# Performance work log

Measured on AMD Instinct MI355X. Metric: run time of the kernel, lower is better.

## Reference

```python
import jax, jax.numpy as jnp
import numpy as np
from jax import lax

P = 10  # patch_size


def _conv(x, w, b, pad):
    y = lax.conv_general_dilated(x, w, (1, 1), [(pad, pad), (pad, pad)],
                                 dimension_numbers=('NCHW', 'OIHW', 'NCHW'))
    return y + b[None, :, None, None]


def setup_inputs() -> dict:
    key = jax.random.key(0)
    ks = jax.random.split(key, 9)
    B, Cin, H, W = 8, 3, 320, 320
    classes = 2
    p2 = P * P
    s = 0.05
    return {
        'x': jax.random.normal(ks[0], (B, Cin, H, W), jnp.float32),
        'w_conv1': jax.random.normal(ks[1], (64, Cin, 7, 7), jnp.float32) * s,
        'b_conv1': jax.random.normal(ks[2], (64,), jnp.float32) * s,
        'w_conv2': jax.random.normal(ks[3], (classes, 64, 3, 3), jnp.float32) * s,
        'b_conv2': jax.random.normal(ks[4], (classes,), jnp.float32) * s,
        'w_fm': jax.random.normal(ks[5], (classes, Cin, 1, 1), jnp.float32) * s,
        'b_fm': jax.random.normal(ks[6], (classes,), jnp.float32) * s,
        'w_lin1': jax.random.normal(ks[7], (2 * p2, p2), jnp.float32) * s,  # torch Linear [out,in]
        'w_lin2': jax.random.normal(ks[8], (p2, 2 * p2), jnp.float32) * s,
    }


def reference(x, w_conv1, b_conv1, w_conv2, b_conv2, w_fm, b_fm, w_lin1, w_lin2):
    p = P
    ini = _conv(_conv(x, w_conv1, b_conv1, 3), w_conv2, b_conv2, 1)  # [B,classes,H,W]
    fea = _conv(x, w_fm, b_fm, 0) / 4.0                              # [B,classes,H,W]
    B, C, H, W = ini.shape
    L = (H // p) * (W // p)

    def unfold(t):  # non-overlapping patches: [B,C,H,W] -> [B,C,L,p*p]
        t = t.reshape(B, C, H // p, p, W // p, p)
        return t.transpose(0, 1, 2, 4, 3, 5).reshape(B, C, L, p * p)

    def trans(t):  # Linear(p2->2p2) -> Linear(2p2->p2) -> ReLU, per patch
        h = jnp.einsum('bclp,qp->bclq', t, w_lin1)
        return jax.nn.relu(jnp.einsum('bclq,pq->bclp', h, w_lin2))

    ui = trans(unfold(ini))   # [B,C,L,p2]
    uf = trans(unfold(fea))   # [B,C,L,p2]
    att = jnp.einsum('bclp,bcmp->bclm', ui, uf) / (p * p)  # [B,C,L,L]
    return att
```

## Files before the change

kernel.cpp:

```cpp
#include <hip/hip_runtime.h>

#define WS_M      0
#define WS_K      10000
#define WS_BETA   12646
#define WS_W9     12664
#define WS_BT     13150
#define WS_INI    16384
#define WS_UIT    (16384 + 1638400)
#define WS_UFT    (16384 + 2*1638400)

typedef short bf16x8 __attribute__((ext_vector_type(8)));
typedef float f32x4  __attribute__((ext_vector_type(4)));

__device__ inline ushort f2bf(float f) {
    unsigned u = __float_as_uint(f);
    unsigned r = (u + 0x7fffu + ((u >> 16) & 1u)) >> 16;
    return (ushort)r;
}

__global__ __launch_bounds__(256) void k_prep(const float* __restrict__ wl1,
                                              const float* __restrict__ wl2,
                                              const float* __restrict__ wc1,
                                              const float* __restrict__ bc1,
                                              const float* __restrict__ wc2,
                                              const float* __restrict__ bc2,
                                              float* __restrict__ ws) {
    int blk = blockIdx.x;
    int t = threadIdx.x;
    if (blk < 40) {
        int idx = blk * 256 + t;
        if (idx < 10000) {
            int p = idx / 100, r = idx % 100;
            float s = 0.f;
            for (int q = 0; q < 200; ++q)
                s += wl2[p * 200 + q] * wl1[q * 100 + r];
            ws[WS_M + r * 100 + p] = s;
        }
        return;
    }
    __shared__ float swc1[9408];
    __shared__ float swc2[1152];
    __shared__ float sBeta[18];
    for (int i = t; i < 9408; i += 256) swc1[i] = wc1[i];
    for (int i = t; i < 1152; i += 256) swc2[i] = wc2[i];
    __syncthreads();
    if (blk < 43) {
        int base = (blk - 40) * 882;
        for (int ii = t; ii < 882; ii += 256) {
            int idx = base + ii;
            int v = idx % 7; int t1 = idx / 7;
            int u = t1 % 7;  int t2 = t1 / 7;
            int ci = t2 % 3; int t3 = t2 / 3;
            int b = t3 % 3;  int t4 = t3 / 3;
            int a = t4 % 3;  int c = t4 / 3;
            float s = 0.f;
            for (int c64 = 0; c64 < 64; ++c64)
                s += swc2[((c * 64 + c64) * 3 + a) * 3 + b] *
                     swc1[((c64 * 3 + ci) * 7 + u) * 7 + v];
            ws[WS_K + idx] = s;
        }
        if (blk == 40) {
            if (t < 18) {
                int b = t % 3; int a = (t / 3) % 3; int c = t / 9;
                float s = 0.f;
                for (int c64 = 0; c64 < 64; ++c64)
                    s += swc2[((c * 64 + c64) * 3 + a) * 3 + b] * bc1[c64];
                sBeta[t] = s; ws[WS_BETA + t] = s;
            }
            __syncthreads();
            if (t < 2) {
                float s = bc2[t];
                for (int j2 = 0; j2 < 9; ++j2) s += sBeta[t * 9 + j2];
                ws[WS_BT + t] = s;
            }
        }
    } else {
        int idx = (blk - 43) * 243 + t;
        if (t < 243) {
            int dx = idx % 9; int t1 = idx / 9;
            int dy = t1 % 9;  int t2 = t1 / 9;
            int ci = t2 % 3;  int c = t2 / 3;
            float s = 0.f;
            for (int a = 0; a < 3; ++a) {
                int u = dy - a; if (u < 0 || u > 6) continue;
                for (int b = 0; b < 3; ++b) {
                    int v = dx - b; if (v < 0 || v > 6) continue;
                    for (int c64 = 0; c64 < 64; ++c64)
                        s += swc2[((c * 64 + c64) * 3 + a) * 3 + b] *
                             swc1[((c64 * 3 + ci) * 7 + u) * 7 + v];
                }
            }
            ws[WS_W9 + idx] = s;
        }
    }
}

__global__ __launch_bounds__(256) void k_convb(const float* __restrict__ x,
                                               const float* __restrict__ bc2,
                                               const float* __restrict__ ws,
                                               float* __restrict__ ini) {
    __shared__ float sx[3][40][40];
    int bid = blockIdx.x;
    int t = threadIdx.x;
    if (bid < 800) {
        int b = bid / 100, by = (bid / 10) % 10, bx = bid % 10;
        int gh0 = by * 32, gw0 = bx * 32;
        for (int idx = t; idx < 3 * 40 * 40; idx += 256) {
            int ci = idx / 1600;
            int rem = idx - ci * 1600;
            int rr = rem / 40, cc = rem - rr * 40;
            int gh = gh0 - 4 + rr, gw = gw0 - 4 + cc;
            float v = 0.f;
            if ((unsigned)gh < 320u && (unsigned)gw < 320u)
                v = x[(b * 3 + ci) * 102400 + gh * 320 + gw];
            sx[ci][rr][cc] = v;
        }
        __syncthreads();
        const float* W9g = ws + WS_W9;
        const float* Btg = ws + WS_BT;
        int r = t >> 3, cg = t & 7;
        int h = gh0 + r, w0c = gw0 + cg * 4;
        float acc0[4], acc1[4];
        float bt0 = Btg[0], bt1 = Btg[1];
        #pragma unroll
        for (int j = 0; j < 4; ++j) { acc0[j] = bt0; acc1[j] = bt1; }
        #pragma unroll
        for (int ci = 0; ci < 3; ++ci) {
            #pragma unroll
            for (int dy = 0; dy < 9; ++dy) {
                const float* xr = &sx[ci][r + dy][cg * 4];
                float4 xa = *(const float4*)(xr);
                float4 xb = *(const float4*)(xr + 4);
                float4 xc = *(const float4*)(xr + 8);
                float xv[12] = {xa.x, xa.y, xa.z, xa.w,
                                xb.x, xb.y, xb.z, xb.w,
                                xc.x, xc.y, xc.z, xc.w};
                #pragma unroll
                for (int dx = 0; dx < 9; ++dx) {
                    float w0t = W9g[ci * 81 + dy * 9 + dx];
                    float w1t = W9g[243 + ci * 81 + dy * 9 + dx];
                    #pragma unroll
                    for (int j = 0; j < 4; ++j) {
                        acc0[j] += w0t * xv[dx + j];
                        acc1[j] += w1t * xv[dx + j];
                    }
                }
            }
        }
        size_t obase = (size_t)(b * 2) * 102400 + h * 320 + w0c;
        bool edge = (by == 0) | (by == 9) | (bx == 0) | (bx == 9);
        if (!edge) {
            *(float4*)&ini[obase] = make_float4(acc0[0], acc0[1], acc0[2], acc0[3]);
            *(float4*)&ini[obase + 102400] = make_float4(acc1[0], acc1[1], acc1[2], acc1[3]);
        } else {
            bool rring = (h == 0) | (h == 319);
            #pragma unroll
            for (int j = 0; j < 4; ++j) {
                int w = w0c + j;
                if (!rring && w != 0 && w != 319) {
                    ini[obase + j] = acc0[j];
                    ini[obase + 102400 + j] = acc1[j];
                }
            }
        }
        return;
    }
    int witem = (bid - 800) * 4 + (t >> 6);
    int lane = t & 63;
    int b = witem / 1276, j = witem % 1276;
    int h, w;
    if (j < 320)      { h = 0;           w = j; }
    else if (j < 640) { h = 319;         w = j - 320; }
    else if (j < 958) { h = 1 + j - 640; w = 0; }
    else              { h = 1 + j - 958; w = 319; }
    const float* K    = ws + WS_K;
    const float* Beta = ws + WS_BETA;
    float acc0 = 0.f, acc1 = 0.f;
    #pragma unroll
    for (int rep = 0; rep < 3; ++rep) {
        int e = lane + rep * 64;
        if (e < 189) {
            int a = e / 63;    int rem  = e - a * 63;
            int bb = rem / 21; int rem2 = rem - bb * 21;
            int ci = rem2 / 7; int u = rem2 - ci * 7;
            int hh0 = h + a - 1;
            int ww0 = w + bb - 1;
            bool abv = ((unsigned)hh0 < 320u) & ((unsigned)ww0 < 320u);
            if (abv && ci == 0 && u == 0) {
                acc0 += Beta[a * 3 + bb];
                acc1 += Beta[9 + a * 3 + bb];
            }
            int hx = hh0 + u - 3;
            if (abv && (unsigned)hx < 320u) {
                const float* Kc = K + (a * 9 + bb * 3 + ci) * 49 + u * 7;
                const float* xr = x + (b * 3 + ci) * 102400 + hx * 320;
                #pragma unroll
                for (int v = 0; v < 7; ++v) {
                    int wx = ww0 + v - 3;
                    if ((unsigned)wx < 320u) {
                        float xv = xr[wx];
                        acc0 += Kc[v] * xv;
                        acc1 += Kc[1323 + v] * xv;
                    }
                }
            }
        }
    }
    #pragma unroll
    for (int off = 32; off > 0; off >>= 1) {
        acc0 += __shfl_down(acc0, off, 64);
        acc1 += __shfl_down(acc1, off, 64);
    }
    if (lane == 0) {
        size_t pb = (size_t)(b * 2) * 102400 + h * 320 + w;
        ini[pb] = acc0 + bc2[0];
        ini[pb + 102400] = acc1 + bc2[1];
    }
}

#define SPS 68
__global__ __launch_bounds__(256) void k_trans(const float* __restrict__ ini,
                                               const float* __restrict__ x,
                                               const float* __restrict__ wfm,
                                               const float* __restrict__ bfm,
                                               const float* __restrict__ ws,
                                               ushort* __restrict__ uiL,
                                               ushort* __restrict__ ufL) {
    __shared__ float sM[100 * 50];
    __shared__ float sP[100 * SPS];
    int bc = blockIdx.x;
    int lg = blockIdx.y;
    int zz = blockIdx.z;
    int mode = zz >> 1, pg = zz & 1;
    ushort* outL = mode ? ufL : uiL;
    int t = threadIdx.x;
    const float* Mt = ws + WS_M;
    for (int i = t; i < 5000; i += 256) {
        int r = i / 50, p = i % 50;
        sM[i] = Mt[r * 100 + pg * 50 + p];
    }
    int b = bc >> 1, c = bc & 1;
    int row0 = lg * 20;
    if (mode == 0) {
        for (int e = t; e < 6400; e += 256) {
            int irow = e / 320, col = e % 320;
            int off = (row0 + irow) * 320 + col;
            float val = ini[bc * 102400 + off];
            int li = (irow / 10) * 32 + col / 10;
            int r  = (irow % 10) * 10 + col % 10;
            sP[r * SPS + li] = val;
        }
    } else {
        float wf0 = wfm[c * 3 + 0], wf1 = wfm[c * 3 + 1], wf2 = wfm[c * 3 + 2];
        float bf = bfm[c];
        for (int e = t; e < 6400; e += 256) {
            int irow = e / 320, col = e % 320;
            int off = (row0 + irow) * 320 + col;
            float val = (bf + x[(b * 3 + 0) * 102400 + off] * wf0
                            + x[(b * 3 + 1) * 102400 + off] * wf1
                            + x[(b * 3 + 2) * 102400 + off] * wf2) * 0.25f;
            int li = (irow / 10) * 32 + col / 10;
            int r  = (irow % 10) * 10 + col % 10;
            sP[r * SPS + li] = val;
        }
    }
    if (pg == 1) {
        for (int e = t; e < 64 * 7; e += 256) {
            int l = lg * 64 + e / 7, q = e % 7;
            *(uint2*)&outL[((size_t)bc * 1024 + l) * 128 + 100 + q * 4] = make_uint2(0u, 0u);
        }
    }
    __syncthreads();
    if (t < 200) {
        int py = t / 8;
        int lx = t % 8;
        int p0 = py * 2, lo = lx * 8;
        float acc[2][8];
        #pragma unroll
        for (int i = 0; i < 2; ++i)
            #pragma unroll
            for (int j = 0; j < 8; ++j) acc[i][j] = 0.f;
        for (int r = 0; r < 100; ++r) {
            float2 a  = *(const float2*)&sM[r * 50 + p0];
            float4 b0 = *(const float4*)&sP[r * SPS + lo];
            float4 b1 = *(const float4*)&sP[r * SPS + lo + 4];
            float av[2] = {a.x, a.y};
            float bv[8] = {b0.x, b0.y, b0.z, b0.w, b1.x, b1.y, b1.z, b1.w};
            #pragma unroll
            for (int i = 0; i < 2; ++i)
                #pragma unroll
                for (int j = 0; j < 8; ++j)
                    acc[i][j] += av[i] * bv[j];
        }
        int pbase = pg * 50 + p0;
        #pragma unroll
        for (int j = 0; j < 8; ++j) {
            int l = lg * 64 + lo + j;
            unsigned v0 = f2bf(fmaxf(acc[0][j], 0.f));
            unsigned v1 = f2bf(fmaxf(acc[1][j], 0.f));
            *(unsigned*)&outL[((size_t)bc * 1024 + l) * 128 + pbase] = v0 | (v1 << 16);
        }
    }
}

__global__ __launch_bounds__(256) void k_att(const ushort* __restrict__ ui,
                                             const ushort* __restrict__ uf,
                                             float* __restrict__ out) {
    int bc   = blockIdx.z;
    int row0 = blockIdx.y * 128, col0 = blockIdx.x * 128;
    int wave = threadIdx.x >> 6, lane = threadIdx.x & 63;
    int r0 = row0 + (wave >> 1) * 64;
    int c0 = col0 + (wave & 1) * 64;
    int m = lane & 15, quad = lane >> 4;
    const ushort* ub = ui + (size_t)bc * 1024 * 128;
    const ushort* vb = uf + (size_t)bc * 1024 * 128;
    f32x4 acc[4][4];
    #pragma unroll
    for (int i = 0; i < 4; ++i)
        #pragma unroll
        for (int j = 0; j < 4; ++j)
            acc[i][j] = (f32x4){0.f, 0.f, 0.f, 0.f};
    #pragma unroll
    for (int k0 = 0; k0 < 128; k0 += 32) {
        bf16x8 af[4], bfr[4];
        #pragma unroll
        for (int i = 0; i < 4; ++i)
            af[i] = *(const bf16x8*)&ub[(size_t)(r0 + i * 16 + m) * 128 + k0 + quad * 8];
        #pragma unroll
        for (int j = 0; j < 4; ++j)
            bfr[j] = *(const bf16x8*)&vb[(size_t)(c0 + j * 16 + m) * 128 + k0 + quad * 8];
        #pragma unroll
        for (int i = 0; i < 4; ++i)
            #pragma unroll
            for (int j = 0; j < 4; ++j)
                acc[i][j] = __builtin_amdgcn_mfma_f32_16x16x32_bf16(af[i], bfr[j], acc[i][j], 0, 0, 0);
    }
    #pragma unroll
    for (int i = 0; i < 4; ++i) {
        #pragma unroll
        for (int r = 0; r < 4; ++r) {
            int row = r0 + i * 16 + quad * 4 + r;
            float* o = out + ((size_t)bc * 1024 + row) * 1024;
            #pragma unroll
            for (int j = 0; j < 4; ++j)
                o[c0 + j * 16 + m] = acc[i][j][r] * 0.01f;
        }
    }
}

extern "C" void kernel_launch(void* const* d_in, const int* in_sizes, int n_in,
                              void* d_out, int out_size, void* d_ws, size_t ws_size,
                              hipStream_t stream) {
    const float* x       = (const float*)d_in[0];
    const float* w_conv1 = (const float*)d_in[1];
    const float* b_conv1 = (const float*)d_in[2];
    const float* w_conv2 = (const float*)d_in[3];
    const float* b_conv2 = (const float*)d_in[4];
    const float* w_fm    = (const float*)d_in[5];
    const float* b_fm    = (const float*)d_in[6];
    const float* w_lin1  = (const float*)d_in[7];
    const float* w_lin2  = (const float*)d_in[8];
    float* out = (float*)d_out;
    float* ws  = (float*)d_ws;
    ushort* uiL = (ushort*)(ws + WS_UIT);
    ushort* ufL = (ushort*)(ws + WS_UFT);

    k_prep<<<45, 256, 0, stream>>>(w_lin1, w_lin2, w_conv1, b_conv1, w_conv2, b_conv2, ws);
    k_convb<<<3352, 256, 0, stream>>>(x, b_conv2, ws, ws + WS_INI);
    k_trans<<<dim3(16, 16, 4), 256, 0, stream>>>(ws + WS_INI, x, w_fm, b_fm, ws, uiL, ufL);
    k_att<<<dim3(8, 8, 16), 256, 0, stream>>>(uiL, ufL, out);
}
```

Before: 170.3 us.

## Fuse all stages into one persistent cooperative kernel with grid syncs

Replaces the four-kernel launch sequence with a single persistent cooperative kernel that runs the prep, conv, patch-transform and attention stages in turn, separated by grid-wide barriers. Each stage loops over its work items with a grid-stride loop, and shared memory is shared between stages through a union. The goal is to remove per-launch overhead and inter-kernel gaps. The cost is that grid syncs add their own barrier latency, occupancy is capped at three blocks per CU, and the fewer resident blocks may run some stages with less parallelism. The original kernels stay as a fallback if the cooperative launch fails.

```diff
diff --git a/kernel.cpp b/kernel.cpp
--- a/kernel.cpp
+++ b/kernel.cpp
@@ -1,4 +1,7 @@
 #include <hip/hip_runtime.h>
+#include <hip/hip_cooperative_groups.h>
+
+namespace cg = cooperative_groups;
 
 #define WS_M      0
 #define WS_K      10000
@@ -16,6 +19,341 @@
     unsigned u = __float_as_uint(f);
     unsigned r = (u + 0x7fffu + ((u >> 16) & 1u)) >> 16;
     return (ushort)r;
+}
+
+#define SPS 68
+
+__global__ __launch_bounds__(256, 3) void k_all(
+    const float* __restrict__ x,
+    const float* __restrict__ wl1, const float* __restrict__ wl2,
+    const float* __restrict__ wc1, const float* __restrict__ bc1,
+    const float* __restrict__ wc2, const float* __restrict__ bc2,
+    const float* __restrict__ wfm, const float* __restrict__ bfm,
+    float* __restrict__ ws, float* __restrict__ out)
+{
+    union alignas(16) SMem {
+        struct { float sx[3][40][40]; float sW9[486]; float sBt[2]; } conv;
+        struct { float sM[5000]; float sP[100 * SPS]; } trans;
+        struct { float swc1[9408]; float swc2[1152]; float sBeta[18]; } prep;
+    };
+    __shared__ SMem sm;
+
+    const int blk = blockIdx.x, t = threadIdx.x, nblk = gridDim.x;
+    float*  Mt   = ws + WS_M;
+    float*  Kw   = ws + WS_K;
+    float*  Beta = ws + WS_BETA;
+    float*  W9   = ws + WS_W9;
+    float*  Bt   = ws + WS_BT;
+    float*  ini  = ws + WS_INI;
+    ushort* uiL  = (ushort*)(ws + WS_UIT);
+    ushort* ufL  = (ushort*)(ws + WS_UFT);
+
+    if (blk < 40) {
+        int idx = blk * 256 + t;
+        if (idx < 10000) {
+            int p = idx / 100, r = idx % 100;
+            float s = 0.f;
+            for (int q = 0; q < 200; ++q)
+                s += wl2[p * 200 + q] * wl1[q * 100 + r];
+            Mt[r * 100 + p] = s;
+        }
+    } else if (blk < 45) {
+        for (int i = t; i < 9408; i += 256) sm.prep.swc1[i] = wc1[i];
+        for (int i = t; i < 1152; i += 256) sm.prep.swc2[i] = wc2[i];
+        __syncthreads();
+        if (blk < 43) {
+            int base = (blk - 40) * 882;
+            for (int ii = t; ii < 882; ii += 256) {
+                int idx = base + ii;
+                int v = idx % 7; int t1 = idx / 7;
+                int u = t1 % 7;  int t2 = t1 / 7;
+                int ci = t2 % 3; int t3 = t2 / 3;
+                int b = t3 % 3;  int t4 = t3 / 3;
+                int a = t4 % 3;  int c = t4 / 3;
+                float s = 0.f;
+                for (int c64 = 0; c64 < 64; ++c64)
+                    s += sm.prep.swc2[((c * 64 + c64) * 3 + a) * 3 + b] *
+                         sm.prep.swc1[((c64 * 3 + ci) * 7 + u) * 7 + v];
+                Kw[idx] = s;
+            }
+            if (blk == 40) {
+                if (t < 18) {
+                    int b = t % 3; int a = (t / 3) % 3; int c = t / 9;
+                    float s = 0.f;
+                    for (int c64 = 0; c64 < 64; ++c64)
+                        s += sm.prep.swc2[((c * 64 + c64) * 3 + a) * 3 + b] * bc1[c64];
+                    sm.prep.sBeta[t] = s; Beta[t] = s;
+                }
+                __syncthreads();
+                if (t < 2) {
+                    float s = bc2[t];
+                    for (int j2 = 0; j2 < 9; ++j2) s += sm.prep.sBeta[t * 9 + j2];
+                    Bt[t] = s;
+                }
+            }
+        } else {
+            int idx = (blk - 43) * 243 + t;
+            if (t < 243) {
+                int dx = idx % 9; int t1 = idx / 9;
+                int dy = t1 % 9;  int t2 = t1 / 9;
+                int ci = t2 % 3;  int c = t2 / 3;
+                float s = 0.f;
+                for (int a = 0; a < 3; ++a) {
+                    int u = dy - a; if (u < 0 || u > 6) continue;
+                    for (int b = 0; b < 3; ++b) {
+                        int v = dx - b; if (v < 0 || v > 6) continue;
+                        for (int c64 = 0; c64 < 64; ++c64)
+                            s += sm.prep.swc2[((c * 64 + c64) * 3 + a) * 3 + b] *
+                                 sm.prep.swc1[((c64 * 3 + ci) * 7 + u) * 7 + v];
+                    }
+                }
+                W9[idx] = s;
+            }
+        }
+    }
+    cg::this_grid().sync();
+
+    for (int u = blk; u < 3352; u += nblk) {
+        if (u < 800) {
+            int b = u / 100, by = (u / 10) % 10, bx = u % 10;
+            int gh0 = by * 32, gw0 = bx * 32;
+            __syncthreads();
+            for (int idx = t; idx < 3 * 40 * 40; idx += 256) {
+                int ci = idx / 1600;
+                int rem = idx - ci * 1600;
+                int rr = rem / 40, cc = rem - rr * 40;
+                int gh = gh0 - 4 + rr, gw = gw0 - 4 + cc;
+                float v = 0.f;
+                if ((unsigned)gh < 320u && (unsigned)gw < 320u)
+                    v = x[(b * 3 + ci) * 102400 + gh * 320 + gw];
+                sm.conv.sx[ci][rr][cc] = v;
+            }
+            for (int i = t; i < 486; i += 256) sm.conv.sW9[i] = W9[i];
+            if (t < 2) sm.conv.sBt[t] = Bt[t];
+            __syncthreads();
+            int r = t >> 3, cg4 = t & 7;
+            int h = gh0 + r, w0c = gw0 + cg4 * 4;
+            float acc0[4], acc1[4];
+            float bt0 = sm.conv.sBt[0], bt1 = sm.conv.sBt[1];
+            #pragma unroll
+            for (int j = 0; j < 4; ++j) { acc0[j] = bt0; acc1[j] = bt1; }
+            #pragma unroll
+            for (int ci = 0; ci < 3; ++ci) {
+                #pragma unroll
+                for (int dy = 0; dy < 9; ++dy) {
+                    const float* xr = &sm.conv.sx[ci][r + dy][cg4 * 4];
+                    float4 xa = *(const float4*)(xr);
+                    float4 xb = *(const float4*)(xr + 4);
+                    float4 xc = *(const float4*)(xr + 8);
+                    float xv[12] = {xa.x, xa.y, xa.z, xa.w,
+                                    xb.x, xb.y, xb.z, xb.w,
+                                    xc.x, xc.y, xc.z, xc.w};
+                    #pragma unroll
+                    for (int dx = 0; dx < 9; ++dx) {
+                        float w0t = sm.conv.sW9[ci * 81 + dy * 9 + dx];
+                        float w1t = sm.conv.sW9[243 + ci * 81 + dy * 9 + dx];
+                        #pragma unroll
+                        for (int j = 0; j < 4; ++j) {
+                            acc0[j] += w0t * xv[dx + j];
+                            acc1[j] += w1t * xv[dx + j];
+                        }
+                    }
+                }
+            }
+            size_t obase = (size_t)(b * 2) * 102400 + h * 320 + w0c;
+            bool edge = (by == 0) | (by == 9) | (bx == 0) | (bx == 9);
+            if (!edge) {
+                *(float4*)&ini[obase] = make_float4(acc0[0], acc0[1], acc0[2], acc0[3]);
+                *(float4*)&ini[obase + 102400] = make_float4(acc1[0], acc1[1], acc1[2], acc1[3]);
+            } else {
+                bool rring = (h == 0) | (h == 319);
+                #pragma unroll
+                for (int j = 0; j < 4; ++j) {
+                    int w = w0c + j;
+                    if (!rring && w != 0 && w != 319) {
+                        ini[obase + j] = acc0[j];
+                        ini[obase + 102400 + j] = acc1[j];
+                    }
+                }
+            }
+        } else {
+            int witem = (u - 800) * 4 + (t >> 6);
+            int lane = t & 63;
+            int b = witem / 1276, j = witem % 1276;
+            int h, w;
+            if (j < 320)      { h = 0;           w = j; }
+            else if (j < 640) { h = 319;         w = j - 320; }
+            else if (j < 958) { h = 1 + j - 640; w = 0; }
+            else              { h = 1 + j - 958; w = 319; }
+            float acc0 = 0.f, acc1 = 0.f;
+            #pragma unroll
+            for (int rep = 0; rep < 3; ++rep) {
+                int e = lane + rep * 64;
+                if (e < 189) {
+                    int a = e / 63;    int rem  = e - a * 63;
+                    int bb = rem / 21; int rem2 = rem - bb * 21;
+                    int ci = rem2 / 7; int uu = rem2 - ci * 7;
+                    int hh0 = h + a - 1;
+                    int ww0 = w + bb - 1;
+                    bool abv = ((unsigned)hh0 < 320u) & ((unsigned)ww0 < 320u);
+                    if (abv && ci == 0 && uu == 0) {
+                        acc0 += Beta[a * 3 + bb];
+                        acc1 += Beta[9 + a * 3 + bb];
+                    }
+                    int hx = hh0 + uu - 3;
+                    if (abv && (unsigned)hx < 320u) {
+                        const float* Kc = Kw + (a * 9 + bb * 3 + ci) * 49 + uu * 7;
+                        const float* xr = x + (b * 3 + ci) * 102400 + hx * 320;
+                        #pragma unroll
+                        for (int v = 0; v < 7; ++v) {
+                            int wx = ww0 + v - 3;
+                            if ((unsigned)wx < 320u) {
+                                float xv = xr[wx];
+                                acc0 += Kc[v] * xv;
+                                acc1 += Kc[1323 + v] * xv;
+                            }
+                        }
+                    }
+                }
+            }
+            #pragma unroll
+            for (int off = 32; off > 0; off >>= 1) {
+                acc0 += __shfl_down(acc0, off, 64);
+                acc1 += __shfl_down(acc1, off, 64);
+            }
+            if (lane == 0) {
+                size_t pb = (size_t)(b * 2) * 102400 + h * 320 + w;
+                ini[pb] = acc0 + bc2[0];
+                ini[pb + 102400] = acc1 + bc2[1];
+            }
+        }
+    }
+    cg::this_grid().sync();
+
+    for (int u = blk; u < 512; u += nblk) {
+        int bc = u & 15, lg = (u >> 4) & 15, mode = u >> 8;
+        ushort* outL = mode ? ufL : uiL;
+        __syncthreads();
+        for (int i = t; i < 5000; i += 256) {
+            int r = i / 50, p = i % 50;
+            sm.trans.sM[i] = Mt[r * 100 + p];
+        }
+        int b = bc >> 1, c = bc & 1;
+        int row0 = lg * 20;
+        if (mode == 0) {
+            for (int e = t; e < 6400; e += 256) {
+                int irow = e / 320, col = e % 320;
+                int off = (row0 + irow) * 320 + col;
+                float val = ini[bc * 102400 + off];
+                int li = (irow / 10) * 32 + col / 10;
+                int r  = (irow % 10) * 10 + col % 10;
+                sm.trans.sP[r * SPS + li] = val;
+            }
+        } else {
+            float wf0 = wfm[c * 3 + 0], wf1 = wfm[c * 3 + 1], wf2 = wfm[c * 3 + 2];
+            float bfv = bfm[c];
+            for (int e = t; e < 6400; e += 256) {
+                int irow = e / 320, col = e % 320;
+                int off = (row0 + irow) * 320 + col;
+                float val = (bfv + x[(b * 3 + 0) * 102400 + off] * wf0
+                                 + x[(b * 3 + 1) * 102400 + off] * wf1
+                                 + x[(b * 3 + 2) * 102400 + off] * wf2) * 0.25f;
+                int li = (irow / 10) * 32 + col / 10;
+                int r  = (irow % 10) * 10 + col % 10;
+                sm.trans.sP[r * SPS + li] = val;
+            }
+        }
+        for (int e = t; e < 64 * 7; e += 256) {
+            int l = lg * 64 + e / 7, q = e % 7;
+            *(uint2*)&outL[((size_t)bc * 1024 + l) * 128 + 100 + q * 4] = make_uint2(0u, 0u);
+        }
+        __syncthreads();
+        auto trans_compute = [&](int pgoff) {
+            if (t < 200) {
+                int py = t / 8, lx = t % 8;
+                int p0 = py * 2, lo = lx * 8;
+                float acc[2][8];
+                #pragma unroll
+                for (int i = 0; i < 2; ++i)
+                    #pragma unroll
+                    for (int j = 0; j < 8; ++j) acc[i][j] = 0.f;
+                for (int r = 0; r < 100; ++r) {
+                    float2 a  = *(const float2*)&sm.trans.sM[r * 50 + p0];
+                    float4 b0 = *(const float4*)&sm.trans.sP[r * SPS + lo];
+                    float4 b1 = *(const float4*)&sm.trans.sP[r * SPS + lo + 4];
+                    float av[2] = {a.x, a.y};
+                    float bv[8] = {b0.x, b0.y, b0.z, b0.w, b1.x, b1.y, b1.z, b1.w};
+                    #pragma unroll
+                    for (int i = 0; i < 2; ++i)
+                        #pragma unroll
+                        for (int j = 0; j < 8; ++j)
+                            acc[i][j] += av[i] * bv[j];
+                }
+                int pbase = pgoff + p0;
+                #pragma unroll
+                for (int j = 0; j < 8; ++j) {
+                    int l = lg * 64 + lo + j;
+                    unsigned v0 = f2bf(fmaxf(acc[0][j], 0.f));
+                    unsigned v1 = f2bf(fmaxf(acc[1][j], 0.f));
+                    *(unsigned*)&outL[((size_t)bc * 1024 + l) * 128 + pbase] = v0 | (v1 << 16);
+                }
+            }
+        };
+        trans_compute(0);
+        __syncthreads();
+        for (int i = t; i < 5000; i += 256) {
+            int r = i / 50, p = i % 50;
+            sm.trans.sM[i] = Mt[r * 100 + 50 + p];
+        }
+        __syncthreads();
+        trans_compute(50);
+    }
+    cg::this_grid().sync();
+
+    for (int u = blk; u < 2048; u += nblk) {
+        int bca  = u >> 7;
+        int rem  = u & 127;
+        int row0 = (rem >> 3) * 64;
+        int col0 = (rem & 7) * 128;
+        int wave = t >> 6, lane = t & 63;
+        int r0 = row0 + (wave >> 1) * 32;
+        int c0 = col0 + (wave & 1) * 64;
+        int m = lane & 15, quad = lane >> 4;
+        const ushort* ub = uiL + (size_t)bca * 131072;
+        const ushort* vb = ufL + (size_t)bca * 131072;
+        f32x4 acc[2][4];
+        #pragma unroll
+        for (int i = 0; i < 2; ++i)
+            #pragma unroll
+            for (int j = 0; j < 4; ++j)
+                acc[i][j] = (f32x4){0.f, 0.f, 0.f, 0.f};
+        #pragma unroll
+        for (int k0 = 0; k0 < 128; k0 += 32) {
+            bf16x8 af[2], bfr[4];
+            #pragma unroll
+            for (int i = 0; i < 2; ++i)
+                af[i] = *(const bf16x8*)&ub[(size_t)(r0 + i * 16 + m) * 128 + k0 + quad * 8];
+            #pragma unroll
+            for (int j = 0; j < 4; ++j)
+                bfr[j] = *(const bf16x8*)&vb[(size_t)(c0 + j * 16 + m) * 128 + k0 + quad * 8];
+            #pragma unroll
+            for (int i = 0; i < 2; ++i)
+                #pragma unroll
+                for (int j = 0; j < 4; ++j)
+                    acc[i][j] = __builtin_amdgcn_mfma_f32_16x16x32_bf16(af[i], bfr[j], acc[i][j], 0, 0, 0);
+        }
+        #pragma unroll
+        for (int i = 0; i < 2; ++i) {
+            #pragma unroll
+            for (int r = 0; r < 4; ++r) {
+                int row = r0 + i * 16 + quad * 4 + r;
+                float* o = out + ((size_t)bca * 1024 + row) * 1024;
+                #pragma unroll
+                for (int j = 0; j < 4; ++j)
+                    o[c0 + j * 16 + m] = acc[i][j][r] * 0.01f;
+            }
+        }
+    }
 }
 
 __global__ __launch_bounds__(256) void k_prep(const float* __restrict__ wl1,
@@ -118,8 +456,8 @@
         __syncthreads();
         const float* W9g = ws + WS_W9;
         const float* Btg = ws + WS_BT;
-        int r = t >> 3, cg = t & 7;
-        int h = gh0 + r, w0c = gw0 + cg * 4;
+        int r = t >> 3, cg4 = t & 7;
+        int h = gh0 + r, w0c = gw0 + cg4 * 4;
         float acc0[4], acc1[4];
         float bt0 = Btg[0], bt1 = Btg[1];
         #pragma unroll
@@ -128,7 +466,7 @@
         for (int ci = 0; ci < 3; ++ci) {
             #pragma unroll
             for (int dy = 0; dy < 9; ++dy) {
-                const float* xr = &sx[ci][r + dy][cg * 4];
+                const float* xr = &sx[ci][r + dy][cg4 * 4];
                 float4 xa = *(const float4*)(xr);
                 float4 xb = *(const float4*)(xr + 4);
                 float4 xc = *(const float4*)(xr + 8);
@@ -218,7 +556,6 @@
     }
 }
 
-#define SPS 68
 __global__ __launch_bounds__(256) void k_trans(const float* __restrict__ ini,
                                                const float* __restrict__ x,
                                                const float* __restrict__ wfm,
@@ -252,13 +589,13 @@
         }
     } else {
         float wf0 = wfm[c * 3 + 0], wf1 = wfm[c * 3 + 1], wf2 = wfm[c * 3 + 2];
-        float bf = bfm[c];
+        float bfv = bfm[c];
         for (int e = t; e < 6400; e += 256) {
             int irow = e / 320, col = e % 320;
             int off = (row0 + irow) * 320 + col;
-            float val = (bf + x[(b * 3 + 0) * 102400 + off] * wf0
-                            + x[(b * 3 + 1) * 102400 + off] * wf1
-                            + x[(b * 3 + 2) * 102400 + off] * wf2) * 0.25f;
+            float val = (bfv + x[(b * 3 + 0) * 102400 + off] * wf0
+                             + x[(b * 3 + 1) * 102400 + off] * wf1
+                             + x[(b * 3 + 2) * 102400 + off] * wf2) * 0.25f;
             int li = (irow / 10) * 32 + col / 10;
             int r  = (irow % 10) * 10 + col % 10;
             sP[r * SPS + li] = val;
@@ -272,8 +609,7 @@
     }
     __syncthreads();
     if (t < 200) {
-        int py = t / 8;
-        int lx = t % 8;
+        int py = t / 8, lx = t % 8;
         int p0 = py * 2, lo = lx * 8;
         float acc[2][8];
         #pragma unroll
@@ -365,8 +701,38 @@
     ushort* uiL = (ushort*)(ws + WS_UIT);
     ushort* ufL = (ushort*)(ws + WS_UFT);
 
-    k_prep<<<45, 256, 0, stream>>>(w_lin1, w_lin2, w_conv1, b_conv1, w_conv2, b_conv2, ws);
-    k_convb<<<3352, 256, 0, stream>>>(x, b_conv2, ws, ws + WS_INI);
-    k_trans<<<dim3(16, 16, 4), 256, 0, stream>>>(ws + WS_INI, x, w_fm, b_fm, ws, uiL, ufL);
-    k_att<<<dim3(8, 8, 16), 256, 0, stream>>>(uiL, ufL, out);
+    static int s_grid = -2;
+    if (s_grid == -2) {
+        int dev = 0;
+        (void)hipGetDevice(&dev);
+        hipDeviceProp_t prop;
+        int ncu = 256;
+        if (hipGetDeviceProperties(&prop, dev) == hipSuccess && prop.multiProcessorCount > 0)
+            ncu = prop.multiProcessorCount;
+        int nb = 0;
+        if (hipOccupancyMaxActiveBlocksPerMultiprocessor(&nb, k_all, 256, 0) != hipSuccess)
+            nb = 0;
+        if (nb > 3) nb = 3;
+        s_grid = (nb > 0) ? nb * ncu : -1;
+    }
+
+    bool done = false;
+    if (s_grid > 0) {
+        void* args[] = {(void*)&x,
+                        (void*)&w_lin1, (void*)&w_lin2,
+                        (void*)&w_conv1, (void*)&b_conv1,
+                        (void*)&w_conv2, (void*)&b_conv2,
+                        (void*)&w_fm, (void*)&b_fm,
+                        (void*)&ws, (void*)&out};
+        hipError_t e = hipLaunchCooperativeKernel(k_all, dim3(s_grid), dim3(256),
+                                                  args, 0u, stream);
+        if (e == hipSuccess) done = true;
+        else s_grid = -1;
+    }
+    if (!done) {
+        k_prep<<<45, 256, 0, stream>>>(w_lin1, w_lin2, w_conv1, b_conv1, w_conv2, b_conv2, ws);
+        k_convb<<<3352, 256, 0, stream>>>(x, b_conv2, ws, ws + WS_INI);
+        k_trans<<<dim3(16, 16, 4), 256, 0, stream>>>(ws + WS_INI, x, w_fm, b_fm, ws, uiL, ufL);
+        k_att<<<dim3(8, 8, 16), 256, 0, stream>>>(uiL, ufL, out);
+    }
 }
```

Result: slower. 323.8 us (+90.1%).

## Fuse folded conv, border fix-up and patch transform into one kernel

Applied to the files above, without the earlier changes.

Replaces the separate conv kernel (which wrote the full ini map to global memory) and the patch-transform kernel with one kernel that processes a 40x40 tile per block. The tile is computed in registers, unfolded into shared memory, and transformed by the folded linear matrix, all without a global round trip for ini. Border pixels are fixed up inside edge blocks from the shared tile. The feature-map path also reuses the staged input. The cost is only 512 blocks, with serialized border work in edge blocks and lower parallelism in the transform phase.

```diff
diff --git a/kernel.cpp b/kernel.cpp
--- a/kernel.cpp
+++ b/kernel.cpp
@@ -5,7 +5,6 @@
 #define WS_BETA   12646
 #define WS_W9     12664
 #define WS_BT     13150
-#define WS_INI    16384
 #define WS_UIT    (16384 + 1638400)
 #define WS_UFT    (16384 + 2*1638400)
 
@@ -95,212 +94,178 @@
     }
 }
 
-__global__ __launch_bounds__(256) void k_convb(const float* __restrict__ x,
-                                               const float* __restrict__ bc2,
-                                               const float* __restrict__ ws,
-                                               float* __restrict__ ini) {
-    __shared__ float sx[3][40][40];
-    int bid = blockIdx.x;
-    int t = threadIdx.x;
-    if (bid < 800) {
-        int b = bid / 100, by = (bid / 10) % 10, bx = bid % 10;
-        int gh0 = by * 32, gw0 = bx * 32;
-        for (int idx = t; idx < 3 * 40 * 40; idx += 256) {
-            int ci = idx / 1600;
-            int rem = idx - ci * 1600;
-            int rr = rem / 40, cc = rem - rr * 40;
-            int gh = gh0 - 4 + rr, gw = gw0 - 4 + cc;
-            float v = 0.f;
-            if ((unsigned)gh < 320u && (unsigned)gw < 320u)
-                v = x[(b * 3 + ci) * 102400 + gh * 320 + gw];
-            sx[ci][rr][cc] = v;
-        }
-        __syncthreads();
-        const float* W9g = ws + WS_W9;
-        const float* Btg = ws + WS_BT;
-        int r = t >> 3, cg = t & 7;
-        int h = gh0 + r, w0c = gw0 + cg * 4;
-        float acc0[4], acc1[4];
-        float bt0 = Btg[0], bt1 = Btg[1];
-        #pragma unroll
-        for (int j = 0; j < 4; ++j) { acc0[j] = bt0; acc1[j] = bt1; }
+__global__ __launch_bounds__(256) void k_fuse(const float* __restrict__ x,
+                                              const float* __restrict__ bc2,
+                                              const float* __restrict__ wfm,
+                                              const float* __restrict__ bfm,
+                                              const float* __restrict__ ws,
+                                              ushort* __restrict__ uiL,
+                                              ushort* __restrict__ ufL) {
+    __shared__ float sx[3][48][52];
+    __shared__ float sP[2][100][20];
+    const int bx = blockIdx.x, by = blockIdx.y, b = blockIdx.z;
+    const int t = threadIdx.x;
+    const float* Mt   = ws + WS_M;
+    const float* Kw   = ws + WS_K;
+    const float* Beta = ws + WS_BETA;
+    const float* W9   = ws + WS_W9;
+    const float* Bt   = ws + WS_BT;
+    const int gh0 = by * 40, gw0 = bx * 40;
+
+    for (int idx = t; idx < 3 * 48 * 48; idx += 256) {
+        int ci = idx / 2304; int rem = idx - ci * 2304;
+        int rr = rem / 48, cc = rem - rr * 48;
+        int gh = gh0 - 4 + rr, gw = gw0 - 4 + cc;
+        float v = 0.f;
+        if ((unsigned)gh < 320u && (unsigned)gw < 320u)
+            v = x[(b * 3 + ci) * 102400 + gh * 320 + gw];
+        sx[ci][rr][cc] = v;
+    }
+    __syncthreads();
+
+    const int lh = t / 5, lw0 = (t % 5) * 8;
+    if (t < 200) {
+        float acc0[8], acc1[8];
+        float bt0 = Bt[0], bt1 = Bt[1];
+        #pragma unroll
+        for (int j = 0; j < 8; ++j) { acc0[j] = bt0; acc1[j] = bt1; }
         #pragma unroll
         for (int ci = 0; ci < 3; ++ci) {
             #pragma unroll
             for (int dy = 0; dy < 9; ++dy) {
-                const float* xr = &sx[ci][r + dy][cg * 4];
+                const float* xr = &sx[ci][lh + dy][lw0];
                 float4 xa = *(const float4*)(xr);
                 float4 xb = *(const float4*)(xr + 4);
                 float4 xc = *(const float4*)(xr + 8);
-                float xv[12] = {xa.x, xa.y, xa.z, xa.w,
-                                xb.x, xb.y, xb.z, xb.w,
-                                xc.x, xc.y, xc.z, xc.w};
+                float4 xd = *(const float4*)(xr + 12);
+                float xv[16] = {xa.x, xa.y, xa.z, xa.w, xb.x, xb.y, xb.z, xb.w,
+                                xc.x, xc.y, xc.z, xc.w, xd.x, xd.y, xd.z, xd.w};
                 #pragma unroll
                 for (int dx = 0; dx < 9; ++dx) {
-                    float w0t = W9g[ci * 81 + dy * 9 + dx];
-                    float w1t = W9g[243 + ci * 81 + dy * 9 + dx];
+                    float w0t = W9[ci * 81 + dy * 9 + dx];
+                    float w1t = W9[243 + ci * 81 + dy * 9 + dx];
                     #pragma unroll
-                    for (int j = 0; j < 4; ++j) {
+                    for (int j = 0; j < 8; ++j) {
                         acc0[j] += w0t * xv[dx + j];
                         acc1[j] += w1t * xv[dx + j];
                     }
                 }
             }
         }
-        size_t obase = (size_t)(b * 2) * 102400 + h * 320 + w0c;
-        bool edge = (by == 0) | (by == 9) | (bx == 0) | (bx == 9);
-        if (!edge) {
-            *(float4*)&ini[obase] = make_float4(acc0[0], acc0[1], acc0[2], acc0[3]);
-            *(float4*)&ini[obase + 102400] = make_float4(acc1[0], acc1[1], acc1[2], acc1[3]);
-        } else {
-            bool rring = (h == 0) | (h == 319);
-            #pragma unroll
-            for (int j = 0; j < 4; ++j) {
-                int w = w0c + j;
-                if (!rring && w != 0 && w != 319) {
-                    ini[obase + j] = acc0[j];
-                    ini[obase + 102400 + j] = acc1[j];
-                }
-            }
-        }
-        return;
-    }
-    int witem = (bid - 800) * 4 + (t >> 6);
-    int lane = t & 63;
-    int b = witem / 1276, j = witem % 1276;
-    int h, w;
-    if (j < 320)      { h = 0;           w = j; }
-    else if (j < 640) { h = 319;         w = j - 320; }
-    else if (j < 958) { h = 1 + j - 640; w = 0; }
-    else              { h = 1 + j - 958; w = 319; }
-    const float* K    = ws + WS_K;
-    const float* Beta = ws + WS_BETA;
-    float acc0 = 0.f, acc1 = 0.f;
-    #pragma unroll
-    for (int rep = 0; rep < 3; ++rep) {
-        int e = lane + rep * 64;
-        if (e < 189) {
-            int a = e / 63;    int rem  = e - a * 63;
-            int bb = rem / 21; int rem2 = rem - bb * 21;
-            int ci = rem2 / 7; int u = rem2 - ci * 7;
-            int hh0 = h + a - 1;
-            int ww0 = w + bb - 1;
-            bool abv = ((unsigned)hh0 < 320u) & ((unsigned)ww0 < 320u);
-            if (abv && ci == 0 && u == 0) {
-                acc0 += Beta[a * 3 + bb];
-                acc1 += Beta[9 + a * 3 + bb];
-            }
-            int hx = hh0 + u - 3;
-            if (abv && (unsigned)hx < 320u) {
-                const float* Kc = K + (a * 9 + bb * 3 + ci) * 49 + u * 7;
-                const float* xr = x + (b * 3 + ci) * 102400 + hx * 320;
-                #pragma unroll
-                for (int v = 0; v < 7; ++v) {
-                    int wx = ww0 + v - 3;
-                    if ((unsigned)wx < 320u) {
-                        float xv = xr[wx];
-                        acc0 += Kc[v] * xv;
-                        acc1 += Kc[1323 + v] * xv;
+        #pragma unroll
+        for (int j = 0; j < 8; ++j) {
+            int lw = lw0 + j;
+            int li = (lh / 10) * 4 + lw / 10;
+            int r  = (lh % 10) * 10 + lw % 10;
+            sP[0][r][li] = acc0[j];
+            sP[1][r][li] = acc1[j];
+        }
+    }
+    __syncthreads();
+
+    bool edgeblk = (by == 0) | (by == 7) | (bx == 0) | (bx == 7);
+    if (edgeblk) {
+        float b20 = bc2[0], b21 = bc2[1];
+        for (int e = t; e < 1600; e += 256) {
+            int elh = e / 40, elw = e % 40;
+            int h = gh0 + elh, w = gw0 + elw;
+            if (h == 0 || h == 319 || w == 0 || w == 319) {
+                float a0 = b20, a1 = b21;
+                for (int a = 0; a < 3; ++a) {
+                    int hh = h + a - 1;
+                    if ((unsigned)hh >= 320u) continue;
+                    for (int bb = 0; bb < 3; ++bb) {
+                        int wwp = w + bb - 1;
+                        if ((unsigned)wwp >= 320u) continue;
+                        a0 += Beta[a * 3 + bb];
+                        a1 += Beta[9 + a * 3 + bb];
+                        for (int ci = 0; ci < 3; ++ci) {
+                            const float* Kc = Kw + ((a * 3 + bb) * 3 + ci) * 49;
+                            #pragma unroll
+                            for (int u = 0; u < 7; ++u) {
+                                #pragma unroll
+                                for (int v = 0; v < 7; ++v) {
+                                    float xv = sx[ci][elh + a + u][elw + bb + v];
+                                    a0 += Kc[u * 7 + v] * xv;
+                                    a1 += Kc[1323 + u * 7 + v] * xv;
+                                }
+                            }
+                        }
                     }
                 }
-            }
-        }
-    }
-    #pragma unroll
-    for (int off = 32; off > 0; off >>= 1) {
-        acc0 += __shfl_down(acc0, off, 64);
-        acc1 += __shfl_down(acc1, off, 64);
-    }
-    if (lane == 0) {
-        size_t pb = (size_t)(b * 2) * 102400 + h * 320 + w;
-        ini[pb] = acc0 + bc2[0];
-        ini[pb + 102400] = acc1 + bc2[1];
-    }
-}
-
-#define SPS 68
-__global__ __launch_bounds__(256) void k_trans(const float* __restrict__ ini,
-                                               const float* __restrict__ x,
-                                               const float* __restrict__ wfm,
-                                               const float* __restrict__ bfm,
-                                               const float* __restrict__ ws,
-                                               ushort* __restrict__ uiL,
-                                               ushort* __restrict__ ufL) {
-    __shared__ float sM[100 * 50];
-    __shared__ float sP[100 * SPS];
-    int bc = blockIdx.x;
-    int lg = blockIdx.y;
-    int zz = blockIdx.z;
-    int mode = zz >> 1, pg = zz & 1;
-    ushort* outL = mode ? ufL : uiL;
-    int t = threadIdx.x;
-    const float* Mt = ws + WS_M;
-    for (int i = t; i < 5000; i += 256) {
-        int r = i / 50, p = i % 50;
-        sM[i] = Mt[r * 100 + pg * 50 + p];
-    }
-    int b = bc >> 1, c = bc & 1;
-    int row0 = lg * 20;
-    if (mode == 0) {
-        for (int e = t; e < 6400; e += 256) {
-            int irow = e / 320, col = e % 320;
-            int off = (row0 + irow) * 320 + col;
-            float val = ini[bc * 102400 + off];
-            int li = (irow / 10) * 32 + col / 10;
-            int r  = (irow % 10) * 10 + col % 10;
-            sP[r * SPS + li] = val;
-        }
-    } else {
-        float wf0 = wfm[c * 3 + 0], wf1 = wfm[c * 3 + 1], wf2 = wfm[c * 3 + 2];
-        float bf = bfm[c];
-        for (int e = t; e < 6400; e += 256) {
-            int irow = e / 320, col = e % 320;
-            int off = (row0 + irow) * 320 + col;
-            float val = (bf + x[(b * 3 + 0) * 102400 + off] * wf0
-                            + x[(b * 3 + 1) * 102400 + off] * wf1
-                            + x[(b * 3 + 2) * 102400 + off] * wf2) * 0.25f;
-            int li = (irow / 10) * 32 + col / 10;
-            int r  = (irow % 10) * 10 + col % 10;
-            sP[r * SPS + li] = val;
-        }
-    }
-    if (pg == 1) {
-        for (int e = t; e < 64 * 7; e += 256) {
-            int l = lg * 64 + e / 7, q = e % 7;
-            *(uint2*)&outL[((size_t)bc * 1024 + l) * 128 + 100 + q * 4] = make_uint2(0u, 0u);
-        }
-    }
-    __syncthreads();
+                int li = (elh / 10) * 4 + elw / 10;
+                int r  = (elh % 10) * 10 + elw % 10;
+                sP[0][r][li] = a0;
+                sP[1][r][li] = a1;
+            }
+        }
+    }
+    __syncthreads();
+
+    auto trans = [&](ushort* outL) {
+        if (t < 200) {
+            int plane = (t >= 100) ? 1 : 0;
+            int p = t - plane * 100;
+            int bc = b * 2 + plane;
+            float acc[16];
+            #pragma unroll
+            for (int k = 0; k < 16; ++k) acc[k] = 0.f;
+            for (int r = 0; r < 100; ++r) {
+                float m = Mt[r * 100 + p];
+                f32x4 s0 = *(const f32x4*)&sP[plane][r][0];
+                f32x4 s1 = *(const f32x4*)&sP[plane][r][4];
+                f32x4 s2 = *(const f32x4*)&sP[plane][r][8];
+                f32x4 s3 = *(const f32x4*)&sP[plane][r][12];
+                #pragma unroll
+                for (int k = 0; k < 4; ++k) acc[k]      += m * s0[k];
+                #pragma unroll
+                for (int k = 0; k < 4; ++k) acc[4 + k]  += m * s1[k];
+                #pragma unroll
+                for (int k = 0; k < 4; ++k) acc[8 + k]  += m * s2[k];
+                #pragma unroll
+                for (int k = 0; k < 4; ++k) acc[12 + k] += m * s3[k];
+            }
+            #pragma unroll
+            for (int k = 0; k < 16; ++k) {
+                int l = (by * 4 + (k >> 2)) * 32 + bx * 4 + (k & 3);
+                outL[((size_t)bc * 1024 + l) * 128 + p] = f2bf(fmaxf(acc[k], 0.f));
+            }
+        } else {
+            for (int task = t - 200; task < 224; task += 56) {
+                int plane = task / 112; int rem = task % 112;
+                int k = rem / 7, q = rem % 7;
+                int bc = b * 2 + plane;
+                int l = (by * 4 + (k >> 2)) * 32 + bx * 4 + (k & 3);
+                *(uint2*)&outL[((size_t)bc * 1024 + l) * 128 + 100 + q * 4] =
+                    make_uint2(0u, 0u);
+            }
+        }
+    };
+
+    trans(uiL);
+    __syncthreads();
+
     if (t < 200) {
-        int py = t / 8;
-        int lx = t % 8;
-        int p0 = py * 2, lo = lx * 8;
-        float acc[2][8];
-        #pragma unroll
-        for (int i = 0; i < 2; ++i)
-            #pragma unroll
-            for (int j = 0; j < 8; ++j) acc[i][j] = 0.f;
-        for (int r = 0; r < 100; ++r) {
-            float2 a  = *(const float2*)&sM[r * 50 + p0];
-            float4 b0 = *(const float4*)&sP[r * SPS + lo];
-            float4 b1 = *(const float4*)&sP[r * SPS + lo + 4];
-            float av[2] = {a.x, a.y};
-            float bv[8] = {b0.x, b0.y, b0.z, b0.w, b1.x, b1.y, b1.z, b1.w};
-            #pragma unroll
-            for (int i = 0; i < 2; ++i)
-                #pragma unroll
-                for (int j = 0; j < 8; ++j)
-                    acc[i][j] += av[i] * bv[j];
-        }
-        int pbase = pg * 50 + p0;
+        float wf00 = wfm[0], wf01 = wfm[1], wf02 = wfm[2];
+        float wf10 = wfm[3], wf11 = wfm[4], wf12 = wfm[5];
+        float bf0 = bfm[0], bf1 = bfm[1];
         #pragma unroll
         for (int j = 0; j < 8; ++j) {
-            int l = lg * 64 + lo + j;
-            unsigned v0 = f2bf(fmaxf(acc[0][j], 0.f));
-            unsigned v1 = f2bf(fmaxf(acc[1][j], 0.f));
-            *(unsigned*)&outL[((size_t)bc * 1024 + l) * 128 + pbase] = v0 | (v1 << 16);
-        }
-    }
+            int lw = lw0 + j;
+            float s0 = sx[0][4 + lh][4 + lw];
+            float s1 = sx[1][4 + lh][4 + lw];
+            float s2 = sx[2][4 + lh][4 + lw];
+            float v0 = (bf0 + s0 * wf00 + s1 * wf01 + s2 * wf02) * 0.25f;
+            float v1 = (bf1 + s0 * wf10 + s1 * wf11 + s2 * wf12) * 0.25f;
+            int li = (lh / 10) * 4 + lw / 10;
+            int r  = (lh % 10) * 10 + lw % 10;
+            sP[0][r][li] = v0;
+            sP[1][r][li] = v1;
+        }
+    }
+    __syncthreads();
+
+    trans(ufL);
 }
 
 __global__ __launch_bounds__(256) void k_att(const ushort* __restrict__ ui,
@@ -366,7 +331,6 @@
     ushort* ufL = (ushort*)(ws + WS_UFT);
 
     k_prep<<<45, 256, 0, stream>>>(w_lin1, w_lin2, w_conv1, b_conv1, w_conv2, b_conv2, ws);
-    k_convb<<<3352, 256, 0, stream>>>(x, b_conv2, ws, ws + WS_INI);
-    k_trans<<<dim3(16, 16, 4), 256, 0, stream>>>(ws + WS_INI, x, w_fm, b_fm, ws, uiL, ufL);
+    k_fuse<<<dim3(8, 8, 8), 256, 0, stream>>>(x, b_conv2, w_fm, b_fm, ws, uiL, ufL);
     k_att<<<dim3(8, 8, 16), 256, 0, stream>>>(uiL, ufL, out);
 }
```

Measured after the change: 261.9 us. 1.54x slower.
